# Kernel optimization log

Hardware: AMD Instinct MI355X
Metric: run time of the kernel (lower is better)

Reference implementation:

```python
import jax, jax.numpy as jnp
import numpy as np
import math

M = 0.5
S = 30.0
COS_M = math.cos(M)
SIN_M = math.sin(M)


def setup_inputs() -> dict:
    key = jax.random.key(0)
    k1, k2, k3 = jax.random.split(key, 3)
    batch, din, nclass = 512, 512, 100000
    x = jax.random.normal(k1, (batch, din), dtype=jnp.float32)
    # xavier_uniform for weight (out, in)
    limit = math.sqrt(6.0 / (nclass + din))
    w = jax.random.uniform(k2, (nclass, din), dtype=jnp.float32, minval=-limit, maxval=limit)
    target = jax.random.randint(k3, (batch,), 0, nclass, dtype=jnp.int64)
    return {"input": x, "weight": w, "target": target}


def reference(input, weight, target):
    # L2-normalize rows (torch F.normalize uses eps=1e-12 clamp on norm)
    xn = input / jnp.maximum(jnp.linalg.norm(input, axis=1, keepdims=True), 1e-12)
    wn = weight / jnp.maximum(jnp.linalg.norm(weight, axis=1, keepdims=True), 1e-12)
    cosine = xn @ wn.T  # [B, C]
    sine = jnp.sqrt(jnp.maximum(1.0 - cosine * cosine, 0.0))
    phi = cosine * COS_M - sine * SIN_M
    # easy_margin=True
    phi = jnp.where(cosine > 0, phi, cosine)
    one_hot = jax.nn.one_hot(target, cosine.shape[1], dtype=cosine.dtype)  # [B, C]
    logits = S * (one_hot * phi + (1.0 - one_hot) * cosine)
    # cross-entropy with mean reduction
    logp = jax.nn.log_softmax(logits, axis=1)
    nll = -jnp.take_along_axis(logp, target[:, None], axis=1)[:, 0]
    return jnp.mean(nll)
```

## Files before the change

### kernel.cpp

```cpp
#include <hip/hip_runtime.h>
#include <math.h>
#include <stdint.h>

#define BATCH 512
#define DIM 512
#define NCLASS 100000
#define BN 64
#define BK 64
#define NSTEP (DIM / BK)
#define NT ((NCLASS + BN - 1) / BN)
#define S_SCALE 30.0f
#define COSM 0.8775825618903728f
#define SINM 0.4794255386042030f

typedef unsigned short u16;
typedef __attribute__((ext_vector_type(8))) short short8;
typedef __attribute__((ext_vector_type(4))) float floatx4;


__device__ __forceinline__ u16 f2bf(float f) {
    union { float f; unsigned int u; } v;
    v.f = f;
    unsigned int u = v.u;
    u += 0x7fffu + ((u >> 16) & 1u);
    return (u16)(u >> 16);
}

__device__ __forceinline__ void async_cp16(const void* g, void* l) {
    auto gp = reinterpret_cast<const __attribute__((address_space(1))) unsigned int*>(
        reinterpret_cast<uintptr_t>(g));
    auto lp = reinterpret_cast<__attribute__((address_space(3))) unsigned int*>(
        reinterpret_cast<uintptr_t>(l));
    __builtin_amdgcn_global_load_lds(gp, lp, 16, 0, 0);
}

__global__ void xnorm_kernel(const float* __restrict__ x, u16* __restrict__ xn) {
    const int row = blockIdx.x;
    const int t = threadIdx.x;
    const floatx4* xr = (const floatx4*)(x + (size_t)row * DIM);
    floatx4 a = xr[t];
    floatx4 b = xr[t + 64];
    float ss = a[0]*a[0] + a[1]*a[1] + a[2]*a[2] + a[3]*a[3]
             + b[0]*b[0] + b[1]*b[1] + b[2]*b[2] + b[3]*b[3];
#pragma unroll
    for (int d = 1; d < 64; d <<= 1) ss += __shfl_xor(ss, d);
    const float rn = 1.0f / fmaxf(sqrtf(ss), 1e-12f);
    ushort4 ua, ub;
    ua.x = f2bf(a[0]*rn); ua.y = f2bf(a[1]*rn); ua.z = f2bf(a[2]*rn); ua.w = f2bf(a[3]*rn);
    ub.x = f2bf(b[0]*rn); ub.y = f2bf(b[1]*rn); ub.z = f2bf(b[2]*rn); ub.w = f2bf(b[3]*rn);
    u16* orow = xn + (size_t)row * DIM;
    *(ushort4*)(orow + 4*t)       = ua;
    *(ushort4*)(orow + 256 + 4*t) = ub;
}

__global__ void arcface_main(const float* __restrict__ w,
                             const u16* __restrict__ xn,
                             const int* __restrict__ target,
                             float* __restrict__ partials,
                             float* __restrict__ tlogit) {
    __shared__ float fbuf[2][BN * BK];
    __shared__ u16   bbuf[BN * BK];
    __shared__ float ssb[BN];

    const int t = threadIdx.x;
    const int tile = blockIdx.x;
    const int c0 = tile * BN;

    const int wave = t >> 6;
    const int lane = t & 63;
    const int quad = lane >> 4;
    const int nin  = lane & 15;
    const int mbase = wave * 64;

    size_t goff[2];
    int ldsoff[2];
#pragma unroll
    for (int j = 0; j < 2; ++j) {
        const int gi = wave * 128 + j * 64 + lane;
        const int cl = gi >> 4, gq = gi & 15;
        int cls = c0 + cl; if (cls > NCLASS - 1) cls = NCLASS - 1;
        goff[j] = (size_t)cls * (DIM * 4) + (size_t)gq * 16;
        ldsoff[j] = wave * 2048 + j * 1024;
    }
    const char* wbytes = (const char*)w;

#pragma unroll
    for (int j = 0; j < 2; ++j)
        async_cp16(wbytes + goff[j], (char*)&fbuf[0][0] + ldsoff[j]);

    if (t < BN) ssb[t] = 0.f;

    floatx4 acc[4][4];
#pragma unroll
    for (int mi = 0; mi < 4; ++mi)
#pragma unroll
        for (int ni = 0; ni < 4; ++ni) {
            acc[mi][ni][0] = 0.f; acc[mi][ni][1] = 0.f;
            acc[mi][ni][2] = 0.f; acc[mi][ni][3] = 0.f;
        }

    const int scl  = t >> 3;
    const int ssub = t & 7;

    for (int ks = 0; ks < NSTEP; ++ks) {
        const int p = ks & 1;
        __syncthreads();

        {
            const floatx4 f0 = *(const floatx4*)((const char*)&fbuf[p][0] + t * 32);
            const floatx4 f1 = *(const floatx4*)((const char*)&fbuf[p][0] + t * 32 + 16);
            float ss = f0[0]*f0[0] + f0[1]*f0[1] + f0[2]*f0[2] + f0[3]*f0[3]
                     + f1[0]*f1[0] + f1[1]*f1[1] + f1[2]*f1[2] + f1[3]*f1[3];
            ss += __shfl_xor(ss, 1);
            ss += __shfl_xor(ss, 2);
            ss += __shfl_xor(ss, 4);
            short8 br;
            br[0] = (short)f2bf(f0[0]); br[1] = (short)f2bf(f0[1]);
            br[2] = (short)f2bf(f0[2]); br[3] = (short)f2bf(f0[3]);
            br[4] = (short)f2bf(f1[0]); br[5] = (short)f2bf(f1[1]);
            br[6] = (short)f2bf(f1[2]); br[7] = (short)f2bf(f1[3]);
            const int gsw = ssub ^ (scl & 7);
            *(short8*)(&bbuf[scl * BK + gsw * 8]) = br;
            if (ssub == 0) ssb[scl] += ss;
        }
        __syncthreads();

        if (ks + 1 < NSTEP) {
            const size_t so = (size_t)(ks + 1) * (BK * 4);
#pragma unroll
            for (int j = 0; j < 2; ++j)
                async_cp16(wbytes + goff[j] + so, (char*)&fbuf[p ^ 1][0] + ldsoff[j]);
        }

#pragma unroll
        for (int kk = 0; kk < 2; ++kk) {
            short8 a[4], b[4];
            const int kg = ks * BK + kk * 32 + quad * 8;
#pragma unroll
            for (int mi = 0; mi < 4; ++mi)
                a[mi] = *(const short8*)(xn + (size_t)(mbase + mi * 16 + nin) * DIM + kg);
#pragma unroll
            for (int ni = 0; ni < 4; ++ni) {
                const int cl = ni * 16 + nin;
                const int g = kk * 4 + quad;
                const int gsw = g ^ (cl & 7);
                b[ni] = *(const short8*)(&bbuf[cl * BK + gsw * 8]);
            }
#pragma unroll
            for (int mi = 0; mi < 4; ++mi)
#pragma unroll
                for (int ni = 0; ni < 4; ++ni)
                    acc[mi][ni] = __builtin_amdgcn_mfma_f32_16x16x32_bf16(
                        a[mi], b[ni], acc[mi][ni], 0, 0, 0);
        }
    }

    float rns[4];
#pragma unroll
    for (int ni = 0; ni < 4; ++ni)
        rns[ni] = 1.0f / fmaxf(sqrtf(ssb[ni * 16 + nin]), 1e-12f);

#pragma unroll
    for (int mi = 0; mi < 4; ++mi) {
#pragma unroll
        for (int reg = 0; reg < 4; ++reg) {
            const int m = mbase + mi * 16 + quad * 4 + reg;
            const int tg = target[m];
            float psum = 0.f;
#pragma unroll
            for (int ni = 0; ni < 4; ++ni) {
                const int c = c0 + ni * 16 + nin;
                if (c < NCLASS) {
                    const float cosv = acc[mi][ni][reg] * rns[ni];
                    float lg = S_SCALE * cosv;
                    if (c == tg) {
                        const float sine = sqrtf(fmaxf(1.f - cosv * cosv, 0.f));
                        float phi = cosv * COSM - sine * SINM;
                        if (!(cosv > 0.f)) phi = cosv;
                        lg = S_SCALE * phi;
                        tlogit[m] = lg;
                    }
                    psum += __expf(lg - S_SCALE);
                }
            }
            psum += __shfl_xor(psum, 1);
            psum += __shfl_xor(psum, 2);
            psum += __shfl_xor(psum, 4);
            psum += __shfl_xor(psum, 8);
            if (nin == 0)
                partials[(size_t)tile * BATCH + m] = psum;
        }
    }
}

__global__ void reduce_lse(const float* __restrict__ partials,
                           const float* __restrict__ tlogit,
                           float* __restrict__ nll) {
    const int m = blockIdx.x;
    const int t = threadIdx.x;
    float s = 0.f;
    for (int b = t; b < NT; b += 256) s += partials[(size_t)b * BATCH + m];
#pragma unroll
    for (int d = 1; d < 64; d <<= 1) s += __shfl_xor(s, d);
    __shared__ float red[4];
    if ((t & 63) == 0) red[t >> 6] = s;
    __syncthreads();
    if (t == 0) {
        const float tot = red[0] + red[1] + red[2] + red[3];
        nll[m] = (logf(tot) + S_SCALE) - tlogit[m];
    }
}

__global__ void reduce_mean(const float* __restrict__ nll, float* __restrict__ out) {
    const int t = threadIdx.x;
    float s = nll[t];
#pragma unroll
    for (int d = 1; d < 64; d <<= 1) s += __shfl_xor(s, d);
    __shared__ float red[8];
    if ((t & 63) == 0) red[t >> 6] = s;
    __syncthreads();
    if (t == 0) {
        float tot = 0.f;
#pragma unroll
        for (int i = 0; i < 8; ++i) tot += red[i];
        out[0] = tot / (float)BATCH;
    }
}

extern "C" void kernel_launch(void* const* d_in, const int* in_sizes, int n_in,
                              void* d_out, int out_size, void* d_ws, size_t ws_size,
                              hipStream_t stream) {
    const float* x = (const float*)d_in[0];
    const float* w = (const float*)d_in[1];
    const int* target = (const int*)d_in[2];

    char* ws = (char*)d_ws;
    u16* xn         = (u16*)ws;
    float* tlogit   = (float*)(ws + 524288);
    float* nll      = (float*)(ws + 526336);
    float* partials = (float*)(ws + 528384);

    xnorm_kernel<<<BATCH, 64, 0, stream>>>(x, xn);
    arcface_main<<<NT, 512, 0, stream>>>(w, xn, target, partials, tlogit);
    reduce_lse<<<BATCH, 256, 0, stream>>>(partials, tlogit, nll);
    reduce_mean<<<1, 512, 0, stream>>>(nll, (float*)d_out);
}
```

Baseline: 423.9 us.

## Double K-tile depth and use single-buffered LDS staging with wider swizzle

Raises the K-step from 64 to 128, halving the number of K-iterations and barriers. The fp32 weight staging moves from double buffering to a single buffer reused after conversion, so the LDS footprint stays roughly constant. The bf16 swizzle widens to 16 groups, and a launch bound plus a waves-per-EU hint are added. In exchange, each thread converts twice the data per step, and the prefetch now overlaps only the MFMA phase.

```diff
diff --git a/kernel.cpp b/kernel.cpp
--- a/kernel.cpp
+++ b/kernel.cpp
@@ -6,7 +6,7 @@
 #define DIM 512
 #define NCLASS 100000
 #define BN 64
-#define BK 64
+#define BK 128
 #define NSTEP (DIM / BK)
 #define NT ((NCLASS + BN - 1) / BN)
 #define S_SCALE 30.0f
@@ -53,12 +53,13 @@
     *(ushort4*)(orow + 256 + 4*t) = ub;
 }
 
-__global__ void arcface_main(const float* __restrict__ w,
-                             const u16* __restrict__ xn,
-                             const int* __restrict__ target,
-                             float* __restrict__ partials,
-                             float* __restrict__ tlogit) {
-    __shared__ float fbuf[2][BN * BK];
+__global__ __launch_bounds__(512) __attribute__((amdgpu_waves_per_eu(2)))
+void arcface_main(const float* __restrict__ w,
+                  const u16* __restrict__ xn,
+                  const int* __restrict__ target,
+                  float* __restrict__ partials,
+                  float* __restrict__ tlogit) {
+    __shared__ float fbuf[BN * BK];
     __shared__ u16   bbuf[BN * BK];
     __shared__ float ssb[BN];
 
@@ -72,21 +73,24 @@
     const int nin  = lane & 15;
     const int mbase = wave * 64;
 
-    size_t goff[2];
-    int ldsoff[2];
-#pragma unroll
-    for (int j = 0; j < 2; ++j) {
-        const int gi = wave * 128 + j * 64 + lane;
-        const int cl = gi >> 4, gq = gi & 15;
+    const int scl  = t >> 3;
+    const int ssub = t & 7;
+
+    size_t goff[4];
+    int ldsoff[4];
+#pragma unroll
+    for (int j = 0; j < 4; ++j) {
+        const int gi = wave * 256 + j * 64 + lane;
+        const int cl = gi >> 5, gq = gi & 31;
         int cls = c0 + cl; if (cls > NCLASS - 1) cls = NCLASS - 1;
         goff[j] = (size_t)cls * (DIM * 4) + (size_t)gq * 16;
-        ldsoff[j] = wave * 2048 + j * 1024;
+        ldsoff[j] = (wave * 4 + j) * 1024;
     }
     const char* wbytes = (const char*)w;
 
 #pragma unroll
-    for (int j = 0; j < 2; ++j)
-        async_cp16(wbytes + goff[j], (char*)&fbuf[0][0] + ldsoff[j]);
+    for (int j = 0; j < 4; ++j)
+        async_cp16(wbytes + goff[j], (char*)fbuf + ldsoff[j]);
 
     if (t < BN) ssb[t] = 0.f;
 
@@ -99,28 +103,36 @@
             acc[mi][ni][2] = 0.f; acc[mi][ni][3] = 0.f;
         }
 
-    const int scl  = t >> 3;
-    const int ssub = t & 7;
-
     for (int ks = 0; ks < NSTEP; ++ks) {
-        const int p = ks & 1;
         __syncthreads();
 
         {
-            const floatx4 f0 = *(const floatx4*)((const char*)&fbuf[p][0] + t * 32);
-            const floatx4 f1 = *(const floatx4*)((const char*)&fbuf[p][0] + t * 32 + 16);
+            const float* fb = fbuf + scl * BK + ssub * 16;
+            const floatx4 f0 = *(const floatx4*)(fb);
+            const floatx4 f1 = *(const floatx4*)(fb + 4);
+            const floatx4 f2 = *(const floatx4*)(fb + 8);
+            const floatx4 f3 = *(const floatx4*)(fb + 12);
             float ss = f0[0]*f0[0] + f0[1]*f0[1] + f0[2]*f0[2] + f0[3]*f0[3]
-                     + f1[0]*f1[0] + f1[1]*f1[1] + f1[2]*f1[2] + f1[3]*f1[3];
+                     + f1[0]*f1[0] + f1[1]*f1[1] + f1[2]*f1[2] + f1[3]*f1[3]
+                     + f2[0]*f2[0] + f2[1]*f2[1] + f2[2]*f2[2] + f2[3]*f2[3]
+                     + f3[0]*f3[0] + f3[1]*f3[1] + f3[2]*f3[2] + f3[3]*f3[3];
             ss += __shfl_xor(ss, 1);
             ss += __shfl_xor(ss, 2);
             ss += __shfl_xor(ss, 4);
-            short8 br;
-            br[0] = (short)f2bf(f0[0]); br[1] = (short)f2bf(f0[1]);
-            br[2] = (short)f2bf(f0[2]); br[3] = (short)f2bf(f0[3]);
-            br[4] = (short)f2bf(f1[0]); br[5] = (short)f2bf(f1[1]);
-            br[6] = (short)f2bf(f1[2]); br[7] = (short)f2bf(f1[3]);
-            const int gsw = ssub ^ (scl & 7);
-            *(short8*)(&bbuf[scl * BK + gsw * 8]) = br;
+            short8 w0, w1;
+            w0[0] = (short)f2bf(f0[0]); w0[1] = (short)f2bf(f0[1]);
+            w0[2] = (short)f2bf(f0[2]); w0[3] = (short)f2bf(f0[3]);
+            w0[4] = (short)f2bf(f1[0]); w0[5] = (short)f2bf(f1[1]);
+            w0[6] = (short)f2bf(f1[2]); w0[7] = (short)f2bf(f1[3]);
+            w1[0] = (short)f2bf(f2[0]); w1[1] = (short)f2bf(f2[1]);
+            w1[2] = (short)f2bf(f2[2]); w1[3] = (short)f2bf(f2[3]);
+            w1[4] = (short)f2bf(f3[0]); w1[5] = (short)f2bf(f3[1]);
+            w1[6] = (short)f2bf(f3[2]); w1[7] = (short)f2bf(f3[3]);
+            const int sw = scl & 15;
+            const int g0 = (2 * ssub) ^ sw;
+            const int g1 = (2 * ssub + 1) ^ sw;
+            *(short8*)(&bbuf[scl * BK + g0 * 8]) = w0;
+            *(short8*)(&bbuf[scl * BK + g1 * 8]) = w1;
             if (ssub == 0) ssb[scl] += ss;
         }
         __syncthreads();
@@ -128,12 +140,12 @@
         if (ks + 1 < NSTEP) {
             const size_t so = (size_t)(ks + 1) * (BK * 4);
 #pragma unroll
-            for (int j = 0; j < 2; ++j)
-                async_cp16(wbytes + goff[j] + so, (char*)&fbuf[p ^ 1][0] + ldsoff[j]);
-        }
-
-#pragma unroll
-        for (int kk = 0; kk < 2; ++kk) {
+            for (int j = 0; j < 4; ++j)
+                async_cp16(wbytes + goff[j] + so, (char*)fbuf + ldsoff[j]);
+        }
+
+#pragma unroll
+        for (int kk = 0; kk < 4; ++kk) {
             short8 a[4], b[4];
             const int kg = ks * BK + kk * 32 + quad * 8;
 #pragma unroll
@@ -142,9 +154,8 @@
 #pragma unroll
             for (int ni = 0; ni < 4; ++ni) {
                 const int cl = ni * 16 + nin;
-                const int g = kk * 4 + quad;
-                const int gsw = g ^ (cl & 7);
-                b[ni] = *(const short8*)(&bbuf[cl * BK + gsw * 8]);
+                const int g = (kk * 4 + quad) ^ (cl & 15);
+                b[ni] = *(const short8*)(&bbuf[cl * BK + g * 8]);
             }
 #pragma unroll
             for (int mi = 0; mi < 4; ++mi)
```

After: 425.6 us. Within noise of the previous version (+0.4%).
